# Kernel optimization log

Measured on AMD Instinct MI355X. Metric: run time of the kernel, lower is better.

Reference implementation:

```python
import jax, jax.numpy as jnp
import numpy as np

B, MAX_H, MAX_W, D, S, HID = 64, 64, 32, 512, 8, 64


def setup_inputs() -> dict:
    key = jax.random.key(0)
    ks = jax.random.split(key, 7)
    return {
        "canonical": jax.random.normal(ks[0], (S, S, D), jnp.float32) * 0.02,
        "w1": jax.random.normal(ks[1], (2, HID), jnp.float32) * 0.5,
        "b1": jax.random.normal(ks[2], (HID,), jnp.float32) * 0.1,
        "w2": jax.random.normal(ks[3], (HID, D), jnp.float32) * 0.05,
        "b2": jax.random.normal(ks[4], (D,), jnp.float32) * 0.05,
        "batch_size": B,
        "target_h_list": jax.random.randint(ks[5], (B,), 1, MAX_H + 1, jnp.int32),
        "target_w_list": jax.random.randint(ks[6], (B,), 1, MAX_W + 1, jnp.int32),
        "max_h": MAX_H,
        "max_w": MAX_W,
    }


def _axis_coords(sizes, max_len):
    # sizes: [B] clamped lengths; returns normalized coords u in [0,1] at each
    # padded position (torch.linspace(0,1,L) semantics; 0 when L==1). [B, max_len]
    idx = jnp.arange(max_len, dtype=jnp.float32)[None, :]
    L = sizes[:, None].astype(jnp.float32)
    return jnp.where(L > 1, idx / jnp.maximum(L - 1.0, 1.0), 0.0)


def _forward(canonical, w1, b1, w2, b2, target_h_list, target_w_list, max_h, max_w):
    S_ = canonical.shape[0]
    Hs = jnp.clip(target_h_list, 1, max_h)  # [B]
    Ws = jnp.clip(target_w_list, 1, max_w)  # [B]

    u = _axis_coords(Hs, max_h)  # [B, mh]
    v = _axis_coords(Ws, max_w)  # [B, mw]

    # Bilinear resize of canonical grid with align_corners=True:
    # source coord = normalized coord * (S-1)
    sy = jnp.clip(u * (S_ - 1), 0.0, S_ - 1.0)  # [B, mh]
    sx = jnp.clip(v * (S_ - 1), 0.0, S_ - 1.0)  # [B, mw]
    y0 = jnp.floor(sy).astype(jnp.int32)
    x0 = jnp.floor(sx).astype(jnp.int32)
    y1 = jnp.minimum(y0 + 1, S_ - 1)
    x1 = jnp.minimum(x0 + 1, S_ - 1)
    wy = (sy - y0.astype(jnp.float32))[:, :, None, None]  # [B, mh, 1, 1]
    wx = (sx - x0.astype(jnp.float32))[:, None, :, None]  # [B, 1, mw, 1]

    yi0 = y0[:, :, None]  # [B, mh, 1]
    yi1 = y1[:, :, None]
    xi0 = x0[:, None, :]  # [B, 1, mw]
    xi1 = x1[:, None, :]
    q00 = canonical[yi0, xi0]  # [B, mh, mw, D]
    q01 = canonical[yi0, xi1]
    q10 = canonical[yi1, xi0]
    q11 = canonical[yi1, xi1]
    bil = ((1.0 - wy) * ((1.0 - wx) * q00 + wx * q01)
           + wy * ((1.0 - wx) * q10 + wx * q11))  # [B, mh, mw, D]

    # Coordinate refinement MLP on (u, v)
    coords = jnp.stack(
        [jnp.broadcast_to(u[:, :, None], (u.shape[0], max_h, max_w)),
         jnp.broadcast_to(v[:, None, :], (u.shape[0], max_h, max_w))],
        axis=-1)  # [B, mh, mw, 2]
    h = jax.nn.gelu(coords @ w1 + b1, approximate=False)
    delta = h @ w2 + b2  # [B, mh, mw, D]

    mask = ((jnp.arange(max_h)[None, :, None] < Hs[:, None, None])
            & (jnp.arange(max_w)[None, None, :] < Ws[:, None, None]))  # [B, mh, mw]
    queries = jnp.where(mask[..., None], bil + delta, 0.0)
    return queries, mask


def reference(canonical, w1, b1, w2, b2, batch_size, target_h_list,
              target_w_list, max_h, max_w):
    return _forward(canonical, w1, b1, w2, b2, target_h_list, target_w_list,
                    max_h, max_w)
```

## Files before the change

### kernel.cpp

```cpp
#include <hip/hip_runtime.h>
#include <math.h>

#define NB    64
#define MAXH  64
#define MAXW  32
#define DCH   512
#define SS    8
#define HID   64

#define QTOTAL ((size_t)NB * MAXH * MAXW * DCH)

__device__ __forceinline__ float gelu_exact(float x) {
    return 0.5f * x * (1.0f + erff(x * 0.70710678118654752440f));
}

__global__ __launch_bounds__(256) void hgqg_kernel(
    const float* __restrict__ canonical,
    const float* __restrict__ w1,
    const float* __restrict__ b1,
    const float* __restrict__ w2,
    const float* __restrict__ b2,
    const int*   __restrict__ hlist,
    const int*   __restrict__ wlist,
    float* __restrict__ out)
{
    const int blk = blockIdx.x;
    const int b   = blk >> 6;
    const int i   = blk & 63;
    const int t   = threadIdx.x;

    int H = hlist[b]; H = min(max(H, 1), MAXH);
    int W = wlist[b]; W = min(max(W, 1), MAXW);

    float* qrow = out + (size_t)blk * (MAXW * DCH);
    float* mrow = out + QTOTAL + (size_t)blk * MAXW;

    const bool row_active = (i < H);

    if (t < MAXW) {
        mrow[t] = (row_active && t < W) ? 1.0f : 0.0f;
    }

    if (!row_active) {
        float4 z = make_float4(0.f, 0.f, 0.f, 0.f);
        float4* q4 = (float4*)qrow;
        #pragma unroll
        for (int r = 0; r < 16; ++r) q4[t + r * 256] = z;
        return;
    }

    const float u  = (H > 1) ? (float)i / (float)(H - 1) : 0.0f;
    const float sy = fminf(fmaxf(u * 7.0f, 0.0f), 7.0f);
    const int   y0 = (int)floorf(sy);
    const int   y1 = min(y0 + 1, SS - 1);
    const float wy = sy - (float)y0;
    const float winv = (W > 1) ? 1.0f / (float)(W - 1) : 0.0f;

    __shared__ float hsh[MAXW][HID];
    {
        const int j  = t >> 3;
        const int k0 = (t & 7) * 8;
        const float v = (float)j * winv;
        #pragma unroll
        for (int kk = 0; kk < 8; ++kk) {
            const int k = k0 + kk;
            const float x = u * w1[k] + v * w1[HID + k] + b1[k];
            hsh[j][k] = gelu_exact(x);
        }
    }
    __syncthreads();

    const int cid = t & 127;
    const int jg  = t >> 7;
    const float4* can4 = (const float4*)canonical;
    const float4* w2v4 = (const float4*)w2;
    const float4  bb2  = ((const float4*)b2)[cid];

    float4 acc[16];

    #pragma unroll
    for (int s = 0; s < 16; ++s) {
        const int j = jg + 2 * s;
        if (j < W) {
            const float vv  = (float)j * winv;
            const float sx  = fminf(fmaxf(vv * 7.0f, 0.0f), 7.0f);
            const float fx0 = floorf(sx);
            const int   x0  = (int)fx0;
            const int   x1  = min(x0 + 1, SS - 1);
            const float wx  = sx - fx0;
            const float4 q00 = can4[(y0 * SS + x0) * 128 + cid];
            const float4 q01 = can4[(y0 * SS + x1) * 128 + cid];
            const float4 q10 = can4[(y1 * SS + x0) * 128 + cid];
            const float4 q11 = can4[(y1 * SS + x1) * 128 + cid];
            float4 t0, t1, bil;
            t0.x = q00.x + wx * (q01.x - q00.x);
            t0.y = q00.y + wx * (q01.y - q00.y);
            t0.z = q00.z + wx * (q01.z - q00.z);
            t0.w = q00.w + wx * (q01.w - q00.w);
            t1.x = q10.x + wx * (q11.x - q10.x);
            t1.y = q10.y + wx * (q11.y - q10.y);
            t1.z = q10.z + wx * (q11.z - q10.z);
            t1.w = q10.w + wx * (q11.w - q10.w);
            bil.x = t0.x + wy * (t1.x - t0.x);
            bil.y = t0.y + wy * (t1.y - t0.y);
            bil.z = t0.z + wy * (t1.z - t0.z);
            bil.w = t0.w + wy * (t1.w - t0.w);
            acc[s].x = bil.x + bb2.x;
            acc[s].y = bil.y + bb2.y;
            acc[s].z = bil.z + bb2.z;
            acc[s].w = bil.w + bb2.w;
        } else {
            acc[s] = make_float4(0.f, 0.f, 0.f, 0.f);
        }
    }

    for (int kb = 0; kb < HID; kb += 4) {
        const float4 wa = w2v4[(kb + 0) * 128 + cid];
        const float4 wb = w2v4[(kb + 1) * 128 + cid];
        const float4 wc = w2v4[(kb + 2) * 128 + cid];
        const float4 wd = w2v4[(kb + 3) * 128 + cid];
        #pragma unroll
        for (int s = 0; s < 16; ++s) {
            const int j = jg + 2 * s;
            if (j < W) {
                const float4 h4 = *(const float4*)&hsh[j][kb];
                acc[s].x += h4.x * wa.x + h4.y * wb.x + h4.z * wc.x + h4.w * wd.x;
                acc[s].y += h4.x * wa.y + h4.y * wb.y + h4.z * wc.y + h4.w * wd.y;
                acc[s].z += h4.x * wa.z + h4.y * wb.z + h4.z * wc.z + h4.w * wd.z;
                acc[s].w += h4.x * wa.w + h4.y * wb.w + h4.z * wc.w + h4.w * wd.w;
            }
        }
    }

    float4* q4 = (float4*)qrow;
    #pragma unroll
    for (int s = 0; s < 16; ++s) {
        const int j = jg + 2 * s;
        q4[j * 128 + cid] = acc[s];
    }
}

extern "C" void kernel_launch(void* const* d_in, const int* in_sizes, int n_in,
                              void* d_out, int out_size, void* d_ws, size_t ws_size,
                              hipStream_t stream) {
    const float* canonical = (const float*)d_in[0];
    const float* w1        = (const float*)d_in[1];
    const float* b1        = (const float*)d_in[2];
    const float* w2        = (const float*)d_in[3];
    const float* b2        = (const float*)d_in[4];
    const int*   hlist     = (const int*)d_in[6];
    const int*   wlist     = (const int*)d_in[7];
    float* out = (float*)d_out;

    hgqg_kernel<<<NB * MAXH, 256, 0, stream>>>(
        canonical, w1, b1, w2, b2, hlist, wlist, out);
}
```

Baseline: 315.5 us.

## Pre-interpolate canonical rows in LDS, prefetch w2, use nontemporal stores

Each block now loads the two canonical rows it needs once and blends them along y into shared memory, so the per-column bilinear step only reads two LDS vectors instead of four global ones. The w2 weights are software-prefetched one k-step ahead with the loop kept rolled. All output stores become nontemporal, and the j<W branches are removed from the inner loop, with masking done only at the final store. This trades some redundant MLP work on masked columns for branch-free vector FMAs and lower cache pollution from the large write stream.

After: 338.8 us. 1.07x slower.

```diff
diff --git a/kernel.cpp b/kernel.cpp
--- a/kernel.cpp
+++ b/kernel.cpp
@@ -9,6 +9,8 @@
 #define HID   64
 
 #define QTOTAL ((size_t)NB * MAXH * MAXW * DCH)
+
+typedef float f4 __attribute__((ext_vector_type(4)));
 
 __device__ __forceinline__ float gelu_exact(float x) {
     return 0.5f * x * (1.0f + erff(x * 0.70710678118654752440f));
@@ -32,31 +34,42 @@
     int H = hlist[b]; H = min(max(H, 1), MAXH);
     int W = wlist[b]; W = min(max(W, 1), MAXW);
 
-    float* qrow = out + (size_t)blk * (MAXW * DCH);
-    float* mrow = out + QTOTAL + (size_t)blk * MAXW;
-
-    const bool row_active = (i < H);
+    f4* q4 = (f4*)(out + (size_t)blk * (MAXW * DCH));
 
     if (t < MAXW) {
-        mrow[t] = (row_active && t < W) ? 1.0f : 0.0f;
+        out[QTOTAL + (size_t)blk * MAXW + t] = (i < H && t < W) ? 1.0f : 0.0f;
     }
 
-    if (!row_active) {
-        float4 z = make_float4(0.f, 0.f, 0.f, 0.f);
-        float4* q4 = (float4*)qrow;
+    if (i >= H) {
+        const f4 z = {0.f, 0.f, 0.f, 0.f};
         #pragma unroll
-        for (int r = 0; r < 16; ++r) q4[t + r * 256] = z;
+        for (int r = 0; r < 16; ++r)
+            __builtin_nontemporal_store(z, q4 + t + r * 256);
         return;
     }
 
-    const float u  = (H > 1) ? (float)i / (float)(H - 1) : 0.0f;
-    const float sy = fminf(fmaxf(u * 7.0f, 0.0f), 7.0f);
-    const int   y0 = (int)floorf(sy);
-    const int   y1 = min(y0 + 1, SS - 1);
-    const float wy = sy - (float)y0;
+    const float u    = (H > 1) ? (float)i / (float)(H - 1) : 0.0f;
+    const float sy   = fminf(u * 7.0f, 7.0f);
+    const int   y0   = (int)sy;
+    const int   y1   = min(y0 + 1, SS - 1);
+    const float wy   = sy - (float)y0;
     const float winv = (W > 1) ? 1.0f / (float)(W - 1) : 0.0f;
 
-    __shared__ float hsh[MAXW][HID];
+    __shared__ f4 ri[SS * 128];
+    {
+        const f4* can4 = (const f4*)canonical;
+        #pragma unroll
+        for (int r = 0; r < 4; ++r) {
+            const int idx = t + r * 256;
+            const int x   = idx >> 7;
+            const int c   = idx & 127;
+            const f4 a = can4[(y0 * SS + x) * 128 + c];
+            const f4 d = can4[(y1 * SS + x) * 128 + c];
+            ri[idx] = a + wy * (d - a);
+        }
+    }
+
+    __shared__ __align__(16) float hsh[MAXW][HID];
     {
         const int j  = t >> 3;
         const int k0 = (t & 7) * 8;
@@ -64,79 +77,54 @@
         #pragma unroll
         for (int kk = 0; kk < 8; ++kk) {
             const int k = k0 + kk;
-            const float x = u * w1[k] + v * w1[HID + k] + b1[k];
-            hsh[j][k] = gelu_exact(x);
+            hsh[j][k] = gelu_exact(u * w1[k] + v * w1[HID + k] + b1[k]);
         }
     }
     __syncthreads();
 
     const int cid = t & 127;
     const int jg  = t >> 7;
-    const float4* can4 = (const float4*)canonical;
-    const float4* w2v4 = (const float4*)w2;
-    const float4  bb2  = ((const float4*)b2)[cid];
+    const f4  bb2 = ((const f4*)b2)[cid];
 
-    float4 acc[16];
+    f4 acc[16];
 
     #pragma unroll
     for (int s = 0; s < 16; ++s) {
-        const int j = jg + 2 * s;
-        if (j < W) {
-            const float vv  = (float)j * winv;
-            const float sx  = fminf(fmaxf(vv * 7.0f, 0.0f), 7.0f);
-            const float fx0 = floorf(sx);
-            const int   x0  = (int)fx0;
-            const int   x1  = min(x0 + 1, SS - 1);
-            const float wx  = sx - fx0;
-            const float4 q00 = can4[(y0 * SS + x0) * 128 + cid];
-            const float4 q01 = can4[(y0 * SS + x1) * 128 + cid];
-            const float4 q10 = can4[(y1 * SS + x0) * 128 + cid];
-            const float4 q11 = can4[(y1 * SS + x1) * 128 + cid];
-            float4 t0, t1, bil;
-            t0.x = q00.x + wx * (q01.x - q00.x);
-            t0.y = q00.y + wx * (q01.y - q00.y);
-            t0.z = q00.z + wx * (q01.z - q00.z);
-            t0.w = q00.w + wx * (q01.w - q00.w);
-            t1.x = q10.x + wx * (q11.x - q10.x);
-            t1.y = q10.y + wx * (q11.y - q10.y);
-            t1.z = q10.z + wx * (q11.z - q10.z);
-            t1.w = q10.w + wx * (q11.w - q10.w);
-            bil.x = t0.x + wy * (t1.x - t0.x);
-            bil.y = t0.y + wy * (t1.y - t0.y);
-            bil.z = t0.z + wy * (t1.z - t0.z);
-            bil.w = t0.w + wy * (t1.w - t0.w);
-            acc[s].x = bil.x + bb2.x;
-            acc[s].y = bil.y + bb2.y;
-            acc[s].z = bil.z + bb2.z;
-            acc[s].w = bil.w + bb2.w;
-        } else {
-            acc[s] = make_float4(0.f, 0.f, 0.f, 0.f);
-        }
+        const int   j  = jg + 2 * s;
+        const float v  = (float)j * winv;
+        const float sx = fminf(v * 7.0f, 7.0f);
+        const int   x0 = (int)sx;
+        const int   x1 = min(x0 + 1, SS - 1);
+        const float wx = sx - (float)x0;
+        const f4 f0 = ri[x0 * 128 + cid];
+        const f4 f1 = ri[x1 * 128 + cid];
+        acc[s] = f0 + wx * (f1 - f0) + bb2;
     }
 
+    const f4* wp = (const f4*)w2 + cid;
+    f4 wa = wp[0 * 128], wb = wp[1 * 128], wc = wp[2 * 128], wd = wp[3 * 128];
+    #pragma unroll 1
     for (int kb = 0; kb < HID; kb += 4) {
-        const float4 wa = w2v4[(kb + 0) * 128 + cid];
-        const float4 wb = w2v4[(kb + 1) * 128 + cid];
-        const float4 wc = w2v4[(kb + 2) * 128 + cid];
-        const float4 wd = w2v4[(kb + 3) * 128 + cid];
+        const int kn = (kb + 4 < HID) ? (kb + 4) : kb;
+        const f4 na = wp[(kn + 0) * 128];
+        const f4 nb = wp[(kn + 1) * 128];
+        const f4 nc = wp[(kn + 2) * 128];
+        const f4 nd = wp[(kn + 3) * 128];
         #pragma unroll
         for (int s = 0; s < 16; ++s) {
             const int j = jg + 2 * s;
-            if (j < W) {
-                const float4 h4 = *(const float4*)&hsh[j][kb];
-                acc[s].x += h4.x * wa.x + h4.y * wb.x + h4.z * wc.x + h4.w * wd.x;
-                acc[s].y += h4.x * wa.y + h4.y * wb.y + h4.z * wc.y + h4.w * wd.y;
-                acc[s].z += h4.x * wa.z + h4.y * wb.z + h4.z * wc.z + h4.w * wd.z;
-                acc[s].w += h4.x * wa.w + h4.y * wb.w + h4.z * wc.w + h4.w * wd.w;
-            }
+            const f4 h4 = *(const f4*)&hsh[j][kb];
+            acc[s] += h4.x * wa + h4.y * wb + h4.z * wc + h4.w * wd;
         }
+        wa = na; wb = nb; wc = nc; wd = nd;
     }
 
-    float4* q4 = (float4*)qrow;
+    const f4 z = {0.f, 0.f, 0.f, 0.f};
     #pragma unroll
     for (int s = 0; s < 16; ++s) {
         const int j = jg + 2 * s;
-        q4[j * 128 + cid] = acc[s];
+        const f4 o = (j < W) ? acc[s] : z;
+        __builtin_nontemporal_store(o, q4 + j * 128 + cid);
     }
 }
 
```
